# Optimization experiments

Measured on AMD Instinct MI355X. Metric: run time of the kernel, lower is better.

The kernel has to match this reference:

```python
import jax, jax.numpy as jnp
import numpy as np

HIDDEN_DIM = 400
STACK_DEPTH = 32
BATCH = 1
SEQ_LEN = 8192


def setup_inputs() -> dict:
    key = jax.random.key(0)
    k1, k2, k3 = jax.random.split(key, 3)
    hidden_state = jax.random.normal(k1, (BATCH, SEQ_LEN, HIDDEN_DIM), dtype=jnp.float32)
    # action_predictor: nn.Linear(hidden_dim, 3)
    W_ap = jax.random.normal(k2, (3, HIDDEN_DIM), dtype=jnp.float32) * 0.05
    b_ap = jnp.zeros((3,), dtype=jnp.float32)
    # D: nn.Parameter(torch.randn(1, hidden_dim))
    D = jax.random.normal(k3, (1, HIDDEN_DIM), dtype=jnp.float32)
    return {"hidden_state": hidden_state, "W_ap": W_ap, "b_ap": b_ap, "D": D}


def reference(hidden_state, W_ap, b_ap, D):
    # hidden_state: [B, T, H]
    B, T, H = hidden_state.shape
    # Per-step action probabilities (computed for all t at once): [B, T, 3]
    probs = jax.nn.softmax(jnp.einsum('bth,ah->bta', hidden_state, W_ap) + b_ap, axis=-1)
    # push value: sigmoid(D . h_t), scalar per (b, t) (well-defined at B=1)
    pv = jax.nn.sigmoid(jnp.einsum('bth,h->bt', hidden_state, D[0]))  # [B, T]
    push = jnp.transpose(probs[..., 0])   # [T, B]
    pop_ = jnp.transpose(probs[..., 1])   # [T, B]
    noop = jnp.transpose(probs[..., 2])   # [T, B]
    pv_t = jnp.transpose(pv)              # [T, B]

    stack0 = jnp.zeros((B, STACK_DEPTH, H), dtype=hidden_state.dtype)

    # Net effect of the two aliased in-place shifts (snapshot semantics):
    #   s2[0] = s[1]; s2[i] = s[i] for i >= 1
    # then stack[0] = push*push_val + pop*s2[1] + noop*s2[0]
    #               = push*push_val + (pop+noop)*s[1]
    def step(stack, xs):
        pu, po, no, v = xs  # each [B]
        s1 = stack[:, 1, :]  # [B, H]
        new_top = (pu * v)[:, None] + (po + no)[:, None] * s1  # [B, H]
        new_stack = stack.at[:, 0, :].set(new_top)
        return new_stack, new_stack

    _, stacks = jax.lax.scan(step, stack0, (push, pop_, noop, pv_t))  # [T, B, D, H]
    return jnp.transpose(stacks, (1, 0, 2, 3))  # [B, T, D, H]
```

## Files before the change

### kernel.cpp

```cpp
#include <hip/hip_runtime.h>

#define HDIM  400
#define TLEN  8192
#define DEPTH 32
#define SLICE (DEPTH * HDIM)
#define SLICE4 (SLICE / 4)
#define ROW4   (HDIM / 4)
#define NF4   ((size_t)TLEN * SLICE4)
#define BLOCK 256

__global__ __launch_bounds__(BLOCK) void val_kernel(
    const float* __restrict__ hs,
    const float* __restrict__ W,
    const float* __restrict__ b,
    const float* __restrict__ D,
    float* __restrict__ val)
{
    const int wave = threadIdx.x >> 6;
    const int lane = threadIdx.x & 63;
    const int t = blockIdx.x * (BLOCK / 64) + wave;

    const float* __restrict__ x = hs + (size_t)t * HDIM;

    float a0 = 0.f, a1 = 0.f, a2 = 0.f, ad = 0.f;
    for (int i = lane; i < HDIM; i += 64) {
        float h = x[i];
        a0 += h * W[i];
        a1 += h * W[HDIM + i];
        a2 += h * W[2 * HDIM + i];
        ad += h * D[i];
    }

    #pragma unroll
    for (int off = 32; off > 0; off >>= 1) {
        a0 += __shfl_xor(a0, off);
        a1 += __shfl_xor(a1, off);
        a2 += __shfl_xor(a2, off);
        ad += __shfl_xor(ad, off);
    }

    float l0 = a0 + b[0];
    float l1 = a1 + b[1];
    float l2 = a2 + b[2];
    float m  = fmaxf(l0, fmaxf(l1, l2));
    float e0 = __expf(l0 - m);
    float e1 = __expf(l1 - m);
    float e2 = __expf(l2 - m);
    float p0 = e0 / (e0 + e1 + e2);
    float pv = 1.0f / (1.0f + __expf(-ad));
    float v  = p0 * pv;

    if (lane == 0) val[t] = v;
}

__global__ __launch_bounds__(BLOCK) void fill_kernel(
    const float* __restrict__ val,
    float4* __restrict__ out)
{
    const unsigned stride = gridDim.x * BLOCK;
    for (unsigned g = blockIdx.x * BLOCK + threadIdx.x; g < NF4; g += stride) {
        unsigned t = g / SLICE4;
        unsigned w = g - t * SLICE4;
        float v = 0.f;
        if (w < ROW4) v = val[t];
        out[g] = make_float4(v, v, v, v);
    }
}

extern "C" void kernel_launch(void* const* d_in, const int* in_sizes, int n_in,
                              void* d_out, int out_size, void* d_ws, size_t ws_size,
                              hipStream_t stream) {
    const float* hs = (const float*)d_in[0];
    const float* W  = (const float*)d_in[1];
    const float* b  = (const float*)d_in[2];
    const float* D  = (const float*)d_in[3];
    float* out = (float*)d_out;
    float* val = (float*)d_ws;

    val_kernel<<<TLEN / (BLOCK / 64), BLOCK, 0, stream>>>(hs, W, b, D, val);
    fill_kernel<<<4096, BLOCK, 0, stream>>>(val, (float4*)out);
}
```

Baseline: 422.3 us.

## Fuse value computation and stack fill into one per-timestep kernel

Merges the dot-product/softmax/sigmoid kernel and the output fill kernel into a single kernel with one block per timestep. Each block computes its scalar value with a block-wide reduction, then writes its own 32x400 output slice, top row set to the value and the rest zero, with unrolled float4 stores. This removes a second launch, the workspace round-trip, and the per-element division used for index decoding, at the cost of a __syncthreads before the stores.

```diff
diff --git a/kernel.cpp b/kernel.cpp
--- a/kernel.cpp
+++ b/kernel.cpp
@@ -1,36 +1,34 @@
 #include <hip/hip_runtime.h>
 
-#define HDIM  400
-#define TLEN  8192
-#define DEPTH 32
-#define SLICE (DEPTH * HDIM)
-#define SLICE4 (SLICE / 4)
+#define HDIM   400
+#define TLEN   8192
+#define DEPTH  32
+#define SLICE4 ((DEPTH * HDIM) / 4)
 #define ROW4   (HDIM / 4)
-#define NF4   ((size_t)TLEN * SLICE4)
-#define BLOCK 256
+#define BLOCK  256
 
-__global__ __launch_bounds__(BLOCK) void val_kernel(
+__global__ __launch_bounds__(BLOCK) void fused_kernel(
     const float* __restrict__ hs,
     const float* __restrict__ W,
     const float* __restrict__ b,
     const float* __restrict__ D,
-    float* __restrict__ val)
+    float4* __restrict__ out)
 {
-    const int wave = threadIdx.x >> 6;
-    const int lane = threadIdx.x & 63;
-    const int t = blockIdx.x * (BLOCK / 64) + wave;
+    const int t    = blockIdx.x;
+    const int tid  = threadIdx.x;
+    const int wave = tid >> 6;
+    const int lane = tid & 63;
 
     const float* __restrict__ x = hs + (size_t)t * HDIM;
 
     float a0 = 0.f, a1 = 0.f, a2 = 0.f, ad = 0.f;
-    for (int i = lane; i < HDIM; i += 64) {
+    for (int i = tid; i < HDIM; i += BLOCK) {
         float h = x[i];
-        a0 += h * W[i];
-        a1 += h * W[HDIM + i];
-        a2 += h * W[2 * HDIM + i];
-        ad += h * D[i];
+        a0 = fmaf(h, W[i],            a0);
+        a1 = fmaf(h, W[HDIM + i],     a1);
+        a2 = fmaf(h, W[2 * HDIM + i], a2);
+        ad = fmaf(h, D[i],            ad);
     }
-
     #pragma unroll
     for (int off = 32; off > 0; off >>= 1) {
         a0 += __shfl_xor(a0, off);
@@ -38,6 +36,16 @@
         a2 += __shfl_xor(a2, off);
         ad += __shfl_xor(ad, off);
     }
+    __shared__ float red[4][BLOCK / 64];
+    if (lane == 0) {
+        red[0][wave] = a0; red[1][wave] = a1;
+        red[2][wave] = a2; red[3][wave] = ad;
+    }
+    __syncthreads();
+    a0 = red[0][0] + red[0][1] + red[0][2] + red[0][3];
+    a1 = red[1][0] + red[1][1] + red[1][2] + red[1][3];
+    a2 = red[2][0] + red[2][1] + red[2][2] + red[2][3];
+    ad = red[3][0] + red[3][1] + red[3][2] + red[3][3];
 
     float l0 = a0 + b[0];
     float l1 = a1 + b[1];
@@ -46,25 +54,18 @@
     float e0 = __expf(l0 - m);
     float e1 = __expf(l1 - m);
     float e2 = __expf(l2 - m);
-    float p0 = e0 / (e0 + e1 + e2);
-    float pv = 1.0f / (1.0f + __expf(-ad));
-    float v  = p0 * pv;
+    float v  = (e0 / (e0 + e1 + e2)) / (1.f + __expf(-ad));
 
-    if (lane == 0) val[t] = v;
-}
+    float4* __restrict__ o = out + (size_t)t * SLICE4;
+    const float4 z4 = make_float4(0.f, 0.f, 0.f, 0.f);
+    const float4 v4 = make_float4(v, v, v, v);
 
-__global__ __launch_bounds__(BLOCK) void fill_kernel(
-    const float* __restrict__ val,
-    float4* __restrict__ out)
-{
-    const unsigned stride = gridDim.x * BLOCK;
-    for (unsigned g = blockIdx.x * BLOCK + threadIdx.x; g < NF4; g += stride) {
-        unsigned t = g / SLICE4;
-        unsigned w = g - t * SLICE4;
-        float v = 0.f;
-        if (w < ROW4) v = val[t];
-        out[g] = make_float4(v, v, v, v);
-    }
+    o[tid] = (tid < ROW4) ? v4 : z4;
+    #pragma unroll
+    for (int k = 1; k < SLICE4 / BLOCK; ++k)
+        o[tid + k * BLOCK] = z4;
+    if (tid < SLICE4 - (SLICE4 / BLOCK) * BLOCK)
+        o[tid + (SLICE4 / BLOCK) * BLOCK] = z4;
 }
 
 extern "C" void kernel_launch(void* const* d_in, const int* in_sizes, int n_in,
@@ -74,9 +75,7 @@
     const float* W  = (const float*)d_in[1];
     const float* b  = (const float*)d_in[2];
     const float* D  = (const float*)d_in[3];
-    float* out = (float*)d_out;
-    float* val = (float*)d_ws;
+    float4* out = (float4*)d_out;
 
-    val_kernel<<<TLEN / (BLOCK / 64), BLOCK, 0, stream>>>(hs, W, b, D, val);
-    fill_kernel<<<4096, BLOCK, 0, stream>>>(val, (float4*)out);
+    fused_kernel<<<TLEN, BLOCK, 0, stream>>>(hs, W, b, D, out);
 }
```

After: 434.1 us. 2.8% more time.
